# Kernel optimization log

Measured on AMD Instinct MI355X. Metric: run time of the kernel, lower is better.

## Reference

```python
import jax, jax.numpy as jnp
import numpy as np

B, T, D_IN, P, Q, D_OUT = 128, 1024, 64, 128, 2, 64


def _lstm_layer(x, w_ih, w_hh, b):
    """One LSTM layer, batch_first. x: [B,T,Din], w_ih: [4P,Din], w_hh: [4P,P], b: [4P].
    PyTorch gate order: i, f, g, o."""
    # Precompute input contribution for all timesteps (the big, parallel GEMM).
    gx = jnp.einsum('btd,gd->btg', x, w_ih) + b          # [B,T,4P]
    gx_t = jnp.swapaxes(gx, 0, 1)                        # [T,B,4P] for scan
    p = w_hh.shape[1]
    h0 = jnp.zeros((x.shape[0], p), dtype=x.dtype)
    c0 = jnp.zeros((x.shape[0], p), dtype=x.dtype)

    def step(carry, g_in):
        h, c = carry
        g = g_in + h @ w_hh.T                            # [B,4P]
        i, f, gg, o = jnp.split(g, 4, axis=-1)
        i = jax.nn.sigmoid(i)
        f = jax.nn.sigmoid(f)
        gg = jnp.tanh(gg)
        o = jax.nn.sigmoid(o)
        c = f * c + i * gg
        h = o * jnp.tanh(c)
        return (h, c), h

    _, hs = jax.lax.scan(step, (h0, c0), gx_t)           # hs: [T,B,P]
    return jnp.swapaxes(hs, 0, 1)                        # [B,T,P]


def setup_inputs() -> dict:
    key = jax.random.key(0)
    ks = jax.random.split(key, 8)
    x = jax.random.normal(ks[0], (B, T, D_IN), dtype=jnp.float32)
    # weight_ih: kaiming-normal-ish; weight_hh: orthogonal-ish (random normal is a fine stand-in
    # numerically; init distribution doesn't change the math being tested).
    w_ih0 = jax.random.normal(ks[1], (4 * P, D_IN), dtype=jnp.float32) * (1.0 / np.sqrt(D_IN))
    w_hh0 = jax.random.normal(ks[2], (4 * P, P), dtype=jnp.float32) * (1.0 / np.sqrt(P))
    w_ih1 = jax.random.normal(ks[3], (4 * P, P), dtype=jnp.float32) * (1.0 / np.sqrt(P))
    w_hh1 = jax.random.normal(ks[4], (4 * P, P), dtype=jnp.float32) * (1.0 / np.sqrt(P))
    # biases initialized to zero in the original (bias_ih + bias_hh folded into one per layer
    # would be equivalent math; keep both for faithfulness)
    b_ih = jnp.zeros((Q, 4 * P), dtype=jnp.float32)
    b_hh = jnp.zeros((Q, 4 * P), dtype=jnp.float32)
    fc_w = jax.random.normal(ks[5], (D_OUT, P), dtype=jnp.float32) * np.sqrt(2.0 / P)
    fc_b = jnp.zeros((D_OUT,), dtype=jnp.float32)
    return {"x": x, "w_ih0": w_ih0, "w_hh0": w_hh0, "w_ih1": w_ih1, "w_hh1": w_hh1,
            "b_ih": b_ih, "b_hh": b_hh, "fc_w": fc_w, "fc_b": fc_b}


def reference(x, w_ih0, w_hh0, w_ih1, w_hh1, b_ih, b_hh, fc_w, fc_b):
    h = _lstm_layer(x, w_ih0, w_hh0, b_ih[0] + b_hh[0])   # layer 0: [B,T,P]
    h = _lstm_layer(h, w_ih1, w_hh1, b_ih[1] + b_hh[1])   # layer 1: [B,T,P]
    return jnp.einsum('btp,op->bto', h, fc_w) + fc_b      # [B,T,D_OUT]
```

## Files before the change

kernel.cpp:

```cpp
#include <hip/hip_runtime.h>

#define NT 1024
#define RINGS 256

typedef _Float16 half8 __attribute__((ext_vector_type(8)));
typedef _Float16 half4 __attribute__((ext_vector_type(4)));
typedef float f32x4 __attribute__((ext_vector_type(4)));
typedef unsigned long long u64;
struct U2 { u64 a, b; };

#ifndef __has_builtin
#define __has_builtin(x) 0
#endif

__device__ __forceinline__ f32x4 MFMA(half8 a, half8 b, f32x4 c) {
  return __builtin_amdgcn_mfma_f32_16x16x32_f16(a, b, c, 0, 0, 0);
}
__device__ __forceinline__ float exp2h(float x) {
#if __has_builtin(__builtin_amdgcn_exp2f)
  return __builtin_amdgcn_exp2f(x);
#else
  return exp2f(x);
#endif
}
__device__ __forceinline__ float sigf(float x) {
  return __builtin_amdgcn_rcpf(1.0f + exp2h(x * -1.44269504f));
}
__device__ __forceinline__ float tanhf2(float x) {
  float t = __builtin_amdgcn_rcpf(1.0f + exp2h(x * 2.88539008f));
  return fmaf(-2.0f, t, 1.0f);
}
__device__ __forceinline__ half8 cvt8(float4 c0, float4 c1) {
  half8 hv;
  hv[0] = (_Float16)c0.x; hv[1] = (_Float16)c0.y;
  hv[2] = (_Float16)c0.z; hv[3] = (_Float16)c0.w;
  hv[4] = (_Float16)c1.x; hv[5] = (_Float16)c1.y;
  hv[6] = (_Float16)c1.z; hv[7] = (_Float16)c1.w;
  return hv;
}
__device__ __forceinline__ half8 ldring(const _Float16* p) {
  const u64* q = (const u64*)p;
  U2 uu;
  uu.a = __hip_atomic_load(q, __ATOMIC_RELAXED, __HIP_MEMORY_SCOPE_AGENT);
  uu.b = __hip_atomic_load(q + 1, __ATOMIC_RELAXED, __HIP_MEMORY_SCOPE_AGENT);
  return __builtin_bit_cast(half8, uu);
}
__device__ __forceinline__ unsigned wpoll(unsigned* p, unsigned tgt,
                                          unsigned cached, int l) {
  unsigned c = cached;
  while (c < tgt) {
    unsigned pv = 0;
    if (l == 0)
      pv = __hip_atomic_load(p, __ATOMIC_ACQUIRE, __HIP_MEMORY_SCOPE_AGENT);
    c = (unsigned)__builtin_amdgcn_readfirstlane((int)pv);
    if (c < tgt) __builtin_amdgcn_s_sleep(2);
  }
  return c;
}

__global__ __launch_bounds__(256) void prep_x(const float* __restrict__ x,
                                              _Float16* __restrict__ Xf) {
  int t0 = blockIdx.x * 256 + threadIdx.x;
  int l = t0 & 63;
  int fid = t0 >> 6;
  int kt = fid & 1;
  int t = (fid >> 1) & (NT - 1);
  int g = fid >> 11;
  int bt = g * 16 + (l & 15);
  int kb = kt * 32 + (l >> 4) * 4;
  const float* src = x + ((size_t)bt * NT + (size_t)t) * 64 + kb;
  float4 v0 = *(const float4*)src;
  float4 v1 = *(const float4*)(src + 16);
  *(half8*)(Xf + (size_t)fid * 512 + l * 8) = cvt8(v0, v1);
}

__global__ __launch_bounds__(512, 1) void lstm_main(
    const float* __restrict__ wih0, const float* __restrict__ whh0,
    const float* __restrict__ wih1, const float* __restrict__ whh1,
    const float* __restrict__ bih, const float* __restrict__ bhh,
    const float* __restrict__ fcw, const float* __restrict__ fcb,
    const _Float16* __restrict__ Xf, _Float16* __restrict__ ringH0,
    unsigned* __restrict__ flags, float* __restrict__ out) {
  const int tid = threadIdx.x;
  const int w = tid >> 6, l = tid & 63;
  const int n = l & 15, lg = l >> 4;
  const bool producer = blockIdx.x < 8;
  const int g = blockIdx.x & 7;

  __shared__ _Float16 hfr[2][4][64][8];
  __shared__ _Float16 fcl[4][4][64][8];

  _Float16* ringG = ringH0 + (size_t)g * RINGS * 2048;
  unsigned* prog = flags + g * 16;
  unsigned* cons = flags + (8 + g) * 16;
  const half8 hz = {0, 0, 0, 0, 0, 0, 0, 0};

  if (producer) {
    half8 A[4][6];
    f32x4 bias[4];
#pragma unroll
    for (int q = 0; q < 4; ++q) {
      int row = (w + 8 * q) * 16 + n;
#pragma unroll
      for (int kt = 0; kt < 2; ++kt) {
        const float* wp = wih0 + (size_t)row * 64 + kt * 32 + lg * 4;
        A[q][kt] = cvt8(*(const float4*)wp, *(const float4*)(wp + 16));
      }
#pragma unroll
      for (int kt = 0; kt < 4; ++kt) {
        const float* wp = whh0 + (size_t)row * 128 + kt * 32 + lg * 4;
        A[q][2 + kt] = cvt8(*(const float4*)wp, *(const float4*)(wp + 16));
      }
      int rb = (w + 8 * q) * 16 + lg * 4;
      f32x4 bv;
#pragma unroll
      for (int r = 0; r < 4; ++r) bv[r] = bih[rb + r] + bhh[rb + r];
      bias[q] = bv;
    }
    if (tid < 256) ((half8*)&hfr[1][0][0][0])[tid] = hz;
    const _Float16* XfG = Xf + (size_t)g * NT * 1024;
    half8 x0 = *(const half8*)(XfG + l * 8);
    half8 x1 = *(const half8*)(XfG + 512 + l * 8);
    f32x4 cst = {0.f, 0.f, 0.f, 0.f};
    unsigned Cc = 0;
    __syncthreads();
    for (int s = 0; s < NT; ++s) {
      half8 xn0, xn1;
      if (s + 1 < NT) {
        const _Float16* p = XfG + (size_t)(s + 1) * 1024 + l * 8;
        xn0 = *(const half8*)p;
        xn1 = *(const half8*)(p + 512);
      }
      if (s >= 224 && (s & 31) == 0)
        Cc = wpoll(cons, (unsigned)(s - 192), Cc, l);
      const int rdk = (s + 1) & 1;
      half8 b2 = *(const half8*)&hfr[rdk][0][l][0];
      half8 b3 = *(const half8*)&hfr[rdk][1][l][0];
      half8 b4 = *(const half8*)&hfr[rdk][2][l][0];
      half8 b5 = *(const half8*)&hfr[rdk][3][l][0];
      f32x4 xc0 = {0.f, 0.f, 0.f, 0.f}, xc1 = xc0, xc2 = xc0, xc3 = xc0;
      xc0 = MFMA(A[0][0], x0, xc0); xc1 = MFMA(A[1][0], x0, xc1);
      xc2 = MFMA(A[2][0], x0, xc2); xc3 = MFMA(A[3][0], x0, xc3);
      xc0 = MFMA(A[0][1], x1, xc0); xc1 = MFMA(A[1][1], x1, xc1);
      xc2 = MFMA(A[2][1], x1, xc2); xc3 = MFMA(A[3][1], x1, xc3);
      f32x4 hc0 = bias[0], hc1 = bias[1], hc2 = bias[2], hc3 = bias[3];
      hc0 = MFMA(A[0][2], b2, hc0); hc1 = MFMA(A[1][2], b2, hc1);
      hc2 = MFMA(A[2][2], b2, hc2); hc3 = MFMA(A[3][2], b2, hc3);
      hc0 = MFMA(A[0][3], b3, hc0); hc1 = MFMA(A[1][3], b3, hc1);
      hc2 = MFMA(A[2][3], b3, hc2); hc3 = MFMA(A[3][3], b3, hc3);
      hc0 = MFMA(A[0][4], b4, hc0); hc1 = MFMA(A[1][4], b4, hc1);
      hc2 = MFMA(A[2][4], b4, hc2); hc3 = MFMA(A[3][4], b4, hc3);
      hc0 = MFMA(A[0][5], b5, hc0); hc1 = MFMA(A[1][5], b5, hc1);
      hc2 = MFMA(A[2][5], b5, hc2); hc3 = MFMA(A[3][5], b5, hc3);
      f32x4 acc0 = hc0 + xc0, acc1 = hc1 + xc1;
      f32x4 acc2 = hc2 + xc2, acc3 = hc3 + xc3;
      half4 hh;
#pragma unroll
      for (int r = 0; r < 4; ++r) {
        float iv = sigf(acc0[r]), fv = sigf(acc1[r]);
        float gv = tanhf2(acc2[r]), ov = sigf(acc3[r]);
        cst[r] = fv * cst[r] + iv * gv;
        hh[r] = (_Float16)(ov * tanhf2(cst[r]));
      }
      *(half4*)&hfr[s & 1][w >> 1][l][(w & 1) << 2] = hh;
      {
        u64 uh = __builtin_bit_cast(u64, hh);
        __hip_atomic_store(
            (u64*)(ringG + (size_t)(s & (RINGS - 1)) * 2048 +
                   (w >> 1) * 512 + l * 8 + (w & 1) * 4),
            uh, __ATOMIC_RELAXED, __HIP_MEMORY_SCOPE_AGENT);
      }
      asm volatile("s_waitcnt lgkmcnt(0)" ::: "memory");
      __builtin_amdgcn_sched_barrier(0);
      __builtin_amdgcn_s_barrier();
      __builtin_amdgcn_sched_barrier(0);
      if ((s & 31) == 31) {
        asm volatile("s_waitcnt vmcnt(0)" ::: "memory");
        __builtin_amdgcn_sched_barrier(0);
        __builtin_amdgcn_s_barrier();
        __builtin_amdgcn_sched_barrier(0);
        if (tid == 0)
          __hip_atomic_store(prog, (unsigned)(s + 1), __ATOMIC_RELEASE,
                             __HIP_MEMORY_SCOPE_AGENT);
      }
      x0 = xn0;
      x1 = xn1;
    }
  } else {
    half8 A[4][8];
    f32x4 bias[4], fcbv = {0.f, 0.f, 0.f, 0.f};
#pragma unroll
    for (int q = 0; q < 4; ++q) {
      int row = (w + 8 * q) * 16 + n;
#pragma unroll
      for (int kt = 0; kt < 4; ++kt) {
        const float* wp = wih1 + (size_t)row * 128 + kt * 32 + lg * 4;
        A[q][kt] = cvt8(*(const float4*)wp, *(const float4*)(wp + 16));
      }
#pragma unroll
      for (int kt = 0; kt < 4; ++kt) {
        const float* wp = whh1 + (size_t)row * 128 + kt * 32 + lg * 4;
        A[q][4 + kt] = cvt8(*(const float4*)wp, *(const float4*)(wp + 16));
      }
      int rb = (w + 8 * q) * 16 + lg * 4;
      f32x4 bv;
#pragma unroll
      for (int r = 0; r < 4; ++r)
        bv[r] = bih[512 + rb + r] + bhh[512 + rb + r];
      bias[q] = bv;
    }
    if (w < 4) {
      int frow = (w << 4) + n;
#pragma unroll
      for (int kt = 0; kt < 4; ++kt) {
        const float* wp = fcw + (size_t)frow * 128 + kt * 32 + lg * 4;
        *(half8*)&fcl[w][kt][l][0] =
            cvt8(*(const float4*)wp, *(const float4*)(wp + 16));
      }
      fcbv = *(const f32x4*)(fcb + (w << 4) + lg * 4);
    }
    if (tid < 256) ((half8*)&hfr[1][0][0][0])[tid] = hz;
    float* outG = out + (size_t)((g << 4) + n) * NT * 64 + (w << 4) + lg * 4;
    f32x4 cst = {0.f, 0.f, 0.f, 0.f};
    __syncthreads();
    unsigned Pc = wpoll(prog, 2u, 0u, l);
    half8 hA0 = ldring(ringG + l * 8);
    half8 hA1 = ldring(ringG + 512 + l * 8);
    half8 hA2 = ldring(ringG + 1024 + l * 8);
    half8 hA3 = ldring(ringG + 1536 + l * 8);
    const _Float16* rb1 = ringG + 2048 + l * 8;
    half8 hB0 = ldring(rb1);
    half8 hB1 = ldring(rb1 + 512);
    half8 hB2 = ldring(rb1 + 1024);
    half8 hB3 = ldring(rb1 + 1536);

#define CSTEP(T, C0, C1, C2, C3)                                               \
  {                                                                            \
    const int rdk_ = ((T) + 1) & 1;                                            \
    half8 b4 = *(const half8*)&hfr[rdk_][0][l][0];                             \
    half8 b5 = *(const half8*)&hfr[rdk_][1][l][0];                             \
    half8 b6 = *(const half8*)&hfr[rdk_][2][l][0];                             \
    half8 b7 = *(const half8*)&hfr[rdk_][3][l][0];                             \
                      \
    f32x4 ic0 = {0.f, 0.f, 0.f, 0.f}, ic1 = ic0, ic2 = ic0, ic3 = ic0;         \
    ic0 = MFMA(A[0][0], C0, ic0); ic1 = MFMA(A[1][0], C0, ic1);                \
    ic2 = MFMA(A[2][0], C0, ic2); ic3 = MFMA(A[3][0], C0, ic3);                \
    ic0 = MFMA(A[0][1], C1, ic0); ic1 = MFMA(A[1][1], C1, ic1);                \
    ic2 = MFMA(A[2][1], C1, ic2); ic3 = MFMA(A[3][1], C1, ic3);                \
    ic0 = MFMA(A[0][2], C2, ic0); ic1 = MFMA(A[1][2], C2, ic1);                \
    ic2 = MFMA(A[2][2], C2, ic2); ic3 = MFMA(A[3][2], C2, ic3);                \
    ic0 = MFMA(A[0][3], C3, ic0); ic1 = MFMA(A[1][3], C3, ic1);                \
    ic2 = MFMA(A[2][3], C3, ic2); ic3 = MFMA(A[3][3], C3, ic3);                \
    if ((T) + 2 < NT) {    \
      Pc = wpoll(prog, (unsigned)((T) + 3), Pc, l);                            \
      const _Float16* rb_ =                                                    \
          ringG + (size_t)(((T) + 2) & (RINGS - 1)) * 2048 + l * 8;            \
      C0 = ldring(rb_);        C1 = ldring(rb_ + 512);                         \
      C2 = ldring(rb_ + 1024); C3 = ldring(rb_ + 1536);                        \
    }                                                                          \
                                                   \
    f32x4 hc0 = bias[0], hc1 = bias[1], hc2 = bias[2], hc3 = bias[3];          \
    hc0 = MFMA(A[0][4], b4, hc0); hc1 = MFMA(A[1][4], b4, hc1);                \
    hc2 = MFMA(A[2][4], b4, hc2); hc3 = MFMA(A[3][4], b4, hc3);                \
    hc0 = MFMA(A[0][5], b5, hc0); hc1 = MFMA(A[1][5], b5, hc1);                \
    hc2 = MFMA(A[2][5], b5, hc2); hc3 = MFMA(A[3][5], b5, hc3);                \
    hc0 = MFMA(A[0][6], b6, hc0); hc1 = MFMA(A[1][6], b6, hc1);                \
    hc2 = MFMA(A[2][6], b6, hc2); hc3 = MFMA(A[3][6], b6, hc3);                \
    hc0 = MFMA(A[0][7], b7, hc0); hc1 = MFMA(A[1][7], b7, hc1);                \
    hc2 = MFMA(A[2][7], b7, hc2); hc3 = MFMA(A[3][7], b7, hc3);                \
    if (w < 4) {                           \
      half8 f0 = *(const half8*)&fcl[w][0][l][0];                              \
      half8 f1 = *(const half8*)&fcl[w][1][l][0];                              \
      half8 f2 = *(const half8*)&fcl[w][2][l][0];                              \
      half8 f3 = *(const half8*)&fcl[w][3][l][0];                              \
      f32x4 afc = fcbv;                                                        \
      afc = MFMA(f0, b4, afc); afc = MFMA(f1, b5, afc);                        \
      afc = MFMA(f2, b6, afc); afc = MFMA(f3, b7, afc);                        \
      if ((T) >= 1) *(f32x4*)(outG + (size_t)((T) - 1) * 64) = afc;            \
    }                                                                          \
    f32x4 acc0 = hc0 + ic0, acc1 = hc1 + ic1;                                  \
    f32x4 acc2 = hc2 + ic2, acc3 = hc3 + ic3;                                  \
    half4 hh;                                                                  \
    _Pragma("unroll")                                                          \
    for (int r = 0; r < 4; ++r) {                                              \
      float iv = sigf(acc0[r]), fv = sigf(acc1[r]);                            \
      float gv = tanhf2(acc2[r]), ov = sigf(acc3[r]);                          \
      cst[r] = fv * cst[r] + iv * gv;                                          \
      hh[r] = (_Float16)(ov * tanhf2(cst[r]));                                 \
    }                                                                          \
    *(half4*)&hfr[(T) & 1][w >> 1][l][(w & 1) << 2] = hh;                      \
    if (tid == 0 && ((T) & 31) == 0)                                           \
      __hip_atomic_store(cons, (unsigned)(T), __ATOMIC_RELAXED,                \
                         __HIP_MEMORY_SCOPE_AGENT);                            \
    asm volatile("s_waitcnt lgkmcnt(0)" ::: "memory");                         \
    __builtin_amdgcn_sched_barrier(0);                                         \
    __builtin_amdgcn_s_barrier();             \
    __builtin_amdgcn_sched_barrier(0);                                         \
  }

    for (int t = 0; t < NT; t += 2) {
      CSTEP(t, hA0, hA1, hA2, hA3);
      CSTEP(t + 1, hB0, hB1, hB2, hB3);
    }
#undef CSTEP
    {
      half8 b4 = *(const half8*)&hfr[(NT + 1) & 1][0][l][0];
      half8 b5 = *(const half8*)&hfr[(NT + 1) & 1][1][l][0];
      half8 b6 = *(const half8*)&hfr[(NT + 1) & 1][2][l][0];
      half8 b7 = *(const half8*)&hfr[(NT + 1) & 1][3][l][0];
      if (w < 4) {
        half8 f0 = *(const half8*)&fcl[w][0][l][0];
        half8 f1 = *(const half8*)&fcl[w][1][l][0];
        half8 f2 = *(const half8*)&fcl[w][2][l][0];
        half8 f3 = *(const half8*)&fcl[w][3][l][0];
        f32x4 afc = fcbv;
        afc = MFMA(f0, b4, afc); afc = MFMA(f1, b5, afc);
        afc = MFMA(f2, b6, afc); afc = MFMA(f3, b7, afc);
        *(f32x4*)(outG + (size_t)(NT - 1) * 64) = afc;
      }
    }
  }
}

extern "C" void kernel_launch(void* const* d_in, const int* in_sizes, int n_in,
                              void* d_out, int out_size, void* d_ws, size_t ws_size,
                              hipStream_t stream) {
  const float* x     = (const float*)d_in[0];
  const float* w_ih0 = (const float*)d_in[1];
  const float* w_hh0 = (const float*)d_in[2];
  const float* w_ih1 = (const float*)d_in[3];
  const float* w_hh1 = (const float*)d_in[4];
  const float* b_ih  = (const float*)d_in[5];
  const float* b_hh  = (const float*)d_in[6];
  const float* fc_w  = (const float*)d_in[7];
  const float* fc_b  = (const float*)d_in[8];

  _Float16* Xf   = (_Float16*)d_ws;
  _Float16* ring = (_Float16*)((char*)d_ws + (16u << 20));
  unsigned* flags = (unsigned*)((char*)d_ws + (24u << 20));

  hipMemsetAsync(flags, 0, 4096, stream);
  prep_x<<<4096, 256, 0, stream>>>(x, Xf);
  lstm_main<<<16, 512, 0, stream>>>(w_ih0, w_hh0, w_ih1, w_hh1, b_ih, b_hh,
                                    fc_w, fc_b, Xf, ring, flags,
                                    (float*)d_out);
}
```

Baseline: 1.337 ms.

## Split layer-1 input projection into separate workgroups pipelined via global ring

Adds a third role of 8 workgroups that computes layer-1's input projection (W_ih1·h0 + bias) from the layer-0 ring and writes fp32 gate pre-activations to a new global ring. The layer-1 recurrent workgroups then only do the W_hh1 MFMAs plus FC on the serial critical path. Progress flags are published every 16 steps instead of 32, and ring loads switch from relaxed atomics to plain loads. This shortens the per-step dependency chain of layer 1 at the cost of an extra global round-trip, more flag polling and 8 more workgroups.

```diff
diff --git a/kernel.cpp b/kernel.cpp
--- a/kernel.cpp
+++ b/kernel.cpp
@@ -1,13 +1,13 @@
 #include <hip/hip_runtime.h>
 
 #define NT 1024
-#define RINGS 256
+#define H0S 256
+#define GS 64
 
 typedef _Float16 half8 __attribute__((ext_vector_type(8)));
 typedef _Float16 half4 __attribute__((ext_vector_type(4)));
 typedef float f32x4 __attribute__((ext_vector_type(4)));
 typedef unsigned long long u64;
-struct U2 { u64 a, b; };
 
 #ifndef __has_builtin
 #define __has_builtin(x) 0
@@ -37,13 +37,6 @@
   hv[4] = (_Float16)c1.x; hv[5] = (_Float16)c1.y;
   hv[6] = (_Float16)c1.z; hv[7] = (_Float16)c1.w;
   return hv;
-}
-__device__ __forceinline__ half8 ldring(const _Float16* p) {
-  const u64* q = (const u64*)p;
-  U2 uu;
-  uu.a = __hip_atomic_load(q, __ATOMIC_RELAXED, __HIP_MEMORY_SCOPE_AGENT);
-  uu.b = __hip_atomic_load(q + 1, __ATOMIC_RELAXED, __HIP_MEMORY_SCOPE_AGENT);
-  return __builtin_bit_cast(half8, uu);
 }
 __device__ __forceinline__ unsigned wpoll(unsigned* p, unsigned tgt,
                                           unsigned cached, int l) {
@@ -57,6 +50,18 @@
   }
   return c;
 }
+
+#define DRAIN_BARRIER()                              \
+  asm volatile("s_waitcnt vmcnt(0)" ::: "memory");   \
+  __builtin_amdgcn_sched_barrier(0);                 \
+  __builtin_amdgcn_s_barrier();                      \
+  __builtin_amdgcn_sched_barrier(0)
+
+#define LGKM_BARRIER()                               \
+  asm volatile("s_waitcnt lgkmcnt(0)" ::: "memory"); \
+  __builtin_amdgcn_sched_barrier(0);                 \
+  __builtin_amdgcn_s_barrier();                      \
+  __builtin_amdgcn_sched_barrier(0)
 
 __global__ __launch_bounds__(256) void prep_x(const float* __restrict__ x,
                                               _Float16* __restrict__ Xf) {
@@ -79,23 +84,26 @@
     const float* __restrict__ wih1, const float* __restrict__ whh1,
     const float* __restrict__ bih, const float* __restrict__ bhh,
     const float* __restrict__ fcw, const float* __restrict__ fcb,
-    const _Float16* __restrict__ Xf, _Float16* __restrict__ ringH0,
-    unsigned* __restrict__ flags, float* __restrict__ out) {
+    const _Float16* __restrict__ Xf, _Float16* __restrict__ h0R,
+    float* __restrict__ gyR, unsigned* __restrict__ flags,
+    float* __restrict__ out) {
   const int tid = threadIdx.x;
   const int w = tid >> 6, l = tid & 63;
   const int n = l & 15, lg = l >> 4;
-  const bool producer = blockIdx.x < 8;
+  const int role = blockIdx.x >> 3;
   const int g = blockIdx.x & 7;
 
   __shared__ _Float16 hfr[2][4][64][8];
   __shared__ _Float16 fcl[4][4][64][8];
 
-  _Float16* ringG = ringH0 + (size_t)g * RINGS * 2048;
-  unsigned* prog = flags + g * 16;
-  unsigned* cons = flags + (8 + g) * 16;
+  _Float16* h0G = h0R + (size_t)g * H0S * 2048;
+  float* gyG = gyR + (size_t)g * GS * 8192;
+  unsigned* pP  = flags + (0 * 8 + g) * 16;
+  unsigned* pXY = flags + (1 * 8 + g) * 16;
+  unsigned* pY  = flags + (2 * 8 + g) * 16;
   const half8 hz = {0, 0, 0, 0, 0, 0, 0, 0};
 
-  if (producer) {
+  if (role == 0) {
     half8 A[4][6];
     f32x4 bias[4];
 #pragma unroll
@@ -122,7 +130,7 @@
     half8 x0 = *(const half8*)(XfG + l * 8);
     half8 x1 = *(const half8*)(XfG + 512 + l * 8);
     f32x4 cst = {0.f, 0.f, 0.f, 0.f};
-    unsigned Cc = 0;
+    unsigned XYp = 0;
     __syncthreads();
     for (int s = 0; s < NT; ++s) {
       half8 xn0, xn1;
@@ -132,82 +140,127 @@
         xn1 = *(const half8*)(p + 512);
       }
       if (s >= 224 && (s & 31) == 0)
-        Cc = wpoll(cons, (unsigned)(s - 192), Cc, l);
+        XYp = wpoll(pXY, (unsigned)(s - 192), XYp, l);
       const int rdk = (s + 1) & 1;
       half8 b2 = *(const half8*)&hfr[rdk][0][l][0];
       half8 b3 = *(const half8*)&hfr[rdk][1][l][0];
       half8 b4 = *(const half8*)&hfr[rdk][2][l][0];
       half8 b5 = *(const half8*)&hfr[rdk][3][l][0];
-      f32x4 xc0 = {0.f, 0.f, 0.f, 0.f}, xc1 = xc0, xc2 = xc0, xc3 = xc0;
-      xc0 = MFMA(A[0][0], x0, xc0); xc1 = MFMA(A[1][0], x0, xc1);
-      xc2 = MFMA(A[2][0], x0, xc2); xc3 = MFMA(A[3][0], x0, xc3);
-      xc0 = MFMA(A[0][1], x1, xc0); xc1 = MFMA(A[1][1], x1, xc1);
-      xc2 = MFMA(A[2][1], x1, xc2); xc3 = MFMA(A[3][1], x1, xc3);
-      f32x4 hc0 = bias[0], hc1 = bias[1], hc2 = bias[2], hc3 = bias[3];
-      hc0 = MFMA(A[0][2], b2, hc0); hc1 = MFMA(A[1][2], b2, hc1);
-      hc2 = MFMA(A[2][2], b2, hc2); hc3 = MFMA(A[3][2], b2, hc3);
-      hc0 = MFMA(A[0][3], b3, hc0); hc1 = MFMA(A[1][3], b3, hc1);
-      hc2 = MFMA(A[2][3], b3, hc2); hc3 = MFMA(A[3][3], b3, hc3);
-      hc0 = MFMA(A[0][4], b4, hc0); hc1 = MFMA(A[1][4], b4, hc1);
-      hc2 = MFMA(A[2][4], b4, hc2); hc3 = MFMA(A[3][4], b4, hc3);
-      hc0 = MFMA(A[0][5], b5, hc0); hc1 = MFMA(A[1][5], b5, hc1);
-      hc2 = MFMA(A[2][5], b5, hc2); hc3 = MFMA(A[3][5], b5, hc3);
-      f32x4 acc0 = hc0 + xc0, acc1 = hc1 + xc1;
-      f32x4 acc2 = hc2 + xc2, acc3 = hc3 + xc3;
+      f32x4 a0 = bias[0], a1 = bias[1], a2 = bias[2], a3 = bias[3];
+      a0 = MFMA(A[0][0], x0, a0); a1 = MFMA(A[1][0], x0, a1);
+      a2 = MFMA(A[2][0], x0, a2); a3 = MFMA(A[3][0], x0, a3);
+      a0 = MFMA(A[0][1], x1, a0); a1 = MFMA(A[1][1], x1, a1);
+      a2 = MFMA(A[2][1], x1, a2); a3 = MFMA(A[3][1], x1, a3);
+      a0 = MFMA(A[0][2], b2, a0); a1 = MFMA(A[1][2], b2, a1);
+      a2 = MFMA(A[2][2], b2, a2); a3 = MFMA(A[3][2], b2, a3);
+      a0 = MFMA(A[0][3], b3, a0); a1 = MFMA(A[1][3], b3, a1);
+      a2 = MFMA(A[2][3], b3, a2); a3 = MFMA(A[3][3], b3, a3);
+      a0 = MFMA(A[0][4], b4, a0); a1 = MFMA(A[1][4], b4, a1);
+      a2 = MFMA(A[2][4], b4, a2); a3 = MFMA(A[3][4], b4, a3);
+      a0 = MFMA(A[0][5], b5, a0); a1 = MFMA(A[1][5], b5, a1);
+      a2 = MFMA(A[2][5], b5, a2); a3 = MFMA(A[3][5], b5, a3);
       half4 hh;
 #pragma unroll
       for (int r = 0; r < 4; ++r) {
-        float iv = sigf(acc0[r]), fv = sigf(acc1[r]);
-        float gv = tanhf2(acc2[r]), ov = sigf(acc3[r]);
+        float iv = sigf(a0[r]), fv = sigf(a1[r]);
+        float gv = tanhf2(a2[r]), ov = sigf(a3[r]);
         cst[r] = fv * cst[r] + iv * gv;
         hh[r] = (_Float16)(ov * tanhf2(cst[r]));
       }
       *(half4*)&hfr[s & 1][w >> 1][l][(w & 1) << 2] = hh;
-      {
-        u64 uh = __builtin_bit_cast(u64, hh);
-        __hip_atomic_store(
-            (u64*)(ringG + (size_t)(s & (RINGS - 1)) * 2048 +
-                   (w >> 1) * 512 + l * 8 + (w & 1) * 4),
-            uh, __ATOMIC_RELAXED, __HIP_MEMORY_SCOPE_AGENT);
-      }
-      asm volatile("s_waitcnt lgkmcnt(0)" ::: "memory");
-      __builtin_amdgcn_sched_barrier(0);
-      __builtin_amdgcn_s_barrier();
-      __builtin_amdgcn_sched_barrier(0);
-      if ((s & 31) == 31) {
-        asm volatile("s_waitcnt vmcnt(0)" ::: "memory");
-        __builtin_amdgcn_sched_barrier(0);
-        __builtin_amdgcn_s_barrier();
-        __builtin_amdgcn_sched_barrier(0);
+      *(u64*)(h0G + (size_t)(s & (H0S - 1)) * 2048 + (w >> 1) * 512 + l * 8 +
+              (w & 1) * 4) = __builtin_bit_cast(u64, hh);
+      LGKM_BARRIER();
+      if ((s & 15) == 15) {
+        DRAIN_BARRIER();
         if (tid == 0)
-          __hip_atomic_store(prog, (unsigned)(s + 1), __ATOMIC_RELEASE,
+          __hip_atomic_store(pP, (unsigned)(s + 1), __ATOMIC_RELEASE,
                              __HIP_MEMORY_SCOPE_AGENT);
       }
       x0 = xn0;
       x1 = xn1;
     }
-  } else {
-    half8 A[4][8];
-    f32x4 bias[4], fcbv = {0.f, 0.f, 0.f, 0.f};
+  } else if (role == 1) {
+    half8 Ai[4][4];
+    f32x4 b1v[4];
 #pragma unroll
     for (int q = 0; q < 4; ++q) {
       int row = (w + 8 * q) * 16 + n;
 #pragma unroll
       for (int kt = 0; kt < 4; ++kt) {
         const float* wp = wih1 + (size_t)row * 128 + kt * 32 + lg * 4;
-        A[q][kt] = cvt8(*(const float4*)wp, *(const float4*)(wp + 16));
-      }
+        Ai[q][kt] = cvt8(*(const float4*)wp, *(const float4*)(wp + 16));
+      }
+      int rb = (w + 8 * q) * 16 + lg * 4;
+      f32x4 bv;
+#pragma unroll
+      for (int r = 0; r < 4; ++r)
+        bv[r] = bih[512 + rb + r] + bhh[512 + rb + r];
+      b1v[q] = bv;
+    }
+    unsigned Pp = wpoll(pP, 2u, 0u, l), Yp = 0;
+    const _Float16* hp0 = h0G + l * 8;
+    half8 hA0 = *(const half8*)hp0;
+    half8 hA1 = *(const half8*)(hp0 + 512);
+    half8 hA2 = *(const half8*)(hp0 + 1024);
+    half8 hA3 = *(const half8*)(hp0 + 1536);
+    const _Float16* hp1 = h0G + 2048 + l * 8;
+    half8 hB0 = *(const half8*)hp1;
+    half8 hB1 = *(const half8*)(hp1 + 512);
+    half8 hB2 = *(const half8*)(hp1 + 1024);
+    half8 hB3 = *(const half8*)(hp1 + 1536);
+
+#define XSTEP(U, H0_, H1_, H2_, H3_)                                           \
+  {                                                                            \
+    f32x4 c0 = b1v[0], c1 = b1v[1], c2 = b1v[2], c3 = b1v[3];                  \
+    c0 = MFMA(Ai[0][0], H0_, c0); c1 = MFMA(Ai[1][0], H0_, c1);                \
+    c2 = MFMA(Ai[2][0], H0_, c2); c3 = MFMA(Ai[3][0], H0_, c3);                \
+    c0 = MFMA(Ai[0][1], H1_, c0); c1 = MFMA(Ai[1][1], H1_, c1);                \
+    c2 = MFMA(Ai[2][1], H1_, c2); c3 = MFMA(Ai[3][1], H1_, c3);                \
+    c0 = MFMA(Ai[0][2], H2_, c0); c1 = MFMA(Ai[1][2], H2_, c1);                \
+    c2 = MFMA(Ai[2][2], H2_, c2); c3 = MFMA(Ai[3][2], H2_, c3);                \
+    c0 = MFMA(Ai[0][3], H3_, c0); c1 = MFMA(Ai[1][3], H3_, c1);                \
+    c2 = MFMA(Ai[2][3], H3_, c2); c3 = MFMA(Ai[3][3], H3_, c3);                \
+    float* gp = gyG + (size_t)((U) & (GS - 1)) * 8192;                         \
+    *(f32x4*)(gp + ((0 + w) * 64 + l) * 4) = c0;                               \
+    *(f32x4*)(gp + ((8 + w) * 64 + l) * 4) = c1;                               \
+    *(f32x4*)(gp + ((16 + w) * 64 + l) * 4) = c2;                              \
+    *(f32x4*)(gp + ((24 + w) * 64 + l) * 4) = c3;                              \
+    if ((U) + 2 < NT) {                \
+      Pp = wpoll(pP, (unsigned)((U) + 3), Pp, l);                              \
+      const _Float16* hp_ =                                                    \
+          h0G + (size_t)(((U) + 2) & (H0S - 1)) * 2048 + l * 8;                \
+      H0_ = *(const half8*)hp_;                                                \
+      H1_ = *(const half8*)(hp_ + 512);                                        \
+      H2_ = *(const half8*)(hp_ + 1024);                                       \
+      H3_ = *(const half8*)(hp_ + 1536);                                       \
+    }                                                                          \
+    if (((U) & 15) == 0 && (U) >= 48)       \
+      Yp = wpoll(pY, (unsigned)((U) - 40), Yp, l);                             \
+    if (((U) & 15) == 15) {                                                    \
+      DRAIN_BARRIER();                                                         \
+      if (tid == 0)                                                            \
+        __hip_atomic_store(pXY, (unsigned)((U) + 1), __ATOMIC_RELEASE,         \
+                           __HIP_MEMORY_SCOPE_AGENT);                          \
+    }                                                                          \
+  }
+
+    for (int u = 0; u < NT; u += 2) {
+      XSTEP(u, hA0, hA1, hA2, hA3);
+      XSTEP(u + 1, hB0, hB1, hB2, hB3);
+    }
+#undef XSTEP
+  } else {
+    half8 Ah[4][4];
+    f32x4 fcbv = {0.f, 0.f, 0.f, 0.f};
+#pragma unroll
+    for (int q = 0; q < 4; ++q) {
+      int row = (w + 8 * q) * 16 + n;
 #pragma unroll
       for (int kt = 0; kt < 4; ++kt) {
         const float* wp = whh1 + (size_t)row * 128 + kt * 32 + lg * 4;
-        A[q][4 + kt] = cvt8(*(const float4*)wp, *(const float4*)(wp + 16));
-      }
-      int rb = (w + 8 * q) * 16 + lg * 4;
-      f32x4 bv;
-#pragma unroll
-      for (int r = 0; r < 4; ++r)
-        bv[r] = bih[512 + rb + r] + bhh[512 + rb + r];
-      bias[q] = bv;
+        Ah[q][kt] = cvt8(*(const float4*)wp, *(const float4*)(wp + 16));
+      }
     }
     if (w < 4) {
       int frow = (w << 4) + n;
@@ -223,99 +276,85 @@
     float* outG = out + (size_t)((g << 4) + n) * NT * 64 + (w << 4) + lg * 4;
     f32x4 cst = {0.f, 0.f, 0.f, 0.f};
     __syncthreads();
-    unsigned Pc = wpoll(prog, 2u, 0u, l);
-    half8 hA0 = ldring(ringG + l * 8);
-    half8 hA1 = ldring(ringG + 512 + l * 8);
-    half8 hA2 = ldring(ringG + 1024 + l * 8);
-    half8 hA3 = ldring(ringG + 1536 + l * 8);
-    const _Float16* rb1 = ringG + 2048 + l * 8;
-    half8 hB0 = ldring(rb1);
-    half8 hB1 = ldring(rb1 + 512);
-    half8 hB2 = ldring(rb1 + 1024);
-    half8 hB3 = ldring(rb1 + 1536);
-
-#define CSTEP(T, C0, C1, C2, C3)                                               \
+    unsigned XYp = wpoll(pXY, 2u, 0u, l);
+    f32x4 gA0 = *(const f32x4*)(gyG + ((0 + w) * 64 + l) * 4);
+    f32x4 gA1 = *(const f32x4*)(gyG + ((8 + w) * 64 + l) * 4);
+    f32x4 gA2 = *(const f32x4*)(gyG + ((16 + w) * 64 + l) * 4);
+    f32x4 gA3 = *(const f32x4*)(gyG + ((24 + w) * 64 + l) * 4);
+    const float* g1p = gyG + 8192;
+    f32x4 gB0 = *(const f32x4*)(g1p + ((0 + w) * 64 + l) * 4);
+    f32x4 gB1 = *(const f32x4*)(g1p + ((8 + w) * 64 + l) * 4);
+    f32x4 gB2 = *(const f32x4*)(g1p + ((16 + w) * 64 + l) * 4);
+    f32x4 gB3 = *(const f32x4*)(g1p + ((24 + w) * 64 + l) * 4);
+
+#define YSTEP(T, G0, G1, G2, G3)                                               \
   {                                                                            \
     const int rdk_ = ((T) + 1) & 1;                                            \
-    half8 b4 = *(const half8*)&hfr[rdk_][0][l][0];                             \
-    half8 b5 = *(const half8*)&hfr[rdk_][1][l][0];                             \
-    half8 b6 = *(const half8*)&hfr[rdk_][2][l][0];                             \
-    half8 b7 = *(const half8*)&hfr[rdk_][3][l][0];                             \
-                      \
-    f32x4 ic0 = {0.f, 0.f, 0.f, 0.f}, ic1 = ic0, ic2 = ic0, ic3 = ic0;         \
-    ic0 = MFMA(A[0][0], C0, ic0); ic1 = MFMA(A[1][0], C0, ic1);                \
-    ic2 = MFMA(A[2][0], C0, ic2); ic3 = MFMA(A[3][0], C0, ic3);                \
-    ic0 = MFMA(A[0][1], C1, ic0); ic1 = MFMA(A[1][1], C1, ic1);                \
-    ic2 = MFMA(A[2][1], C1, ic2); ic3 = MFMA(A[3][1], C1, ic3);                \
-    ic0 = MFMA(A[0][2], C2, ic0); ic1 = MFMA(A[1][2], C2, ic1);                \
-    ic2 = MFMA(A[2][2], C2, ic2); ic3 = MFMA(A[3][2], C2, ic3);                \
-    ic0 = MFMA(A[0][3], C3, ic0); ic1 = MFMA(A[1][3], C3, ic1);                \
-    ic2 = MFMA(A[2][3], C3, ic2); ic3 = MFMA(A[3][3], C3, ic3);                \
-    if ((T) + 2 < NT) {    \
-      Pc = wpoll(prog, (unsigned)((T) + 3), Pc, l);                            \
-      const _Float16* rb_ =                                                    \
-          ringG + (size_t)(((T) + 2) & (RINGS - 1)) * 2048 + l * 8;            \
-      C0 = ldring(rb_);        C1 = ldring(rb_ + 512);                         \
-      C2 = ldring(rb_ + 1024); C3 = ldring(rb_ + 1536);                        \
-    }                                                                          \
-                                                   \
-    f32x4 hc0 = bias[0], hc1 = bias[1], hc2 = bias[2], hc3 = bias[3];          \
-    hc0 = MFMA(A[0][4], b4, hc0); hc1 = MFMA(A[1][4], b4, hc1);                \
-    hc2 = MFMA(A[2][4], b4, hc2); hc3 = MFMA(A[3][4], b4, hc3);                \
-    hc0 = MFMA(A[0][5], b5, hc0); hc1 = MFMA(A[1][5], b5, hc1);                \
-    hc2 = MFMA(A[2][5], b5, hc2); hc3 = MFMA(A[3][5], b5, hc3);                \
-    hc0 = MFMA(A[0][6], b6, hc0); hc1 = MFMA(A[1][6], b6, hc1);                \
-    hc2 = MFMA(A[2][6], b6, hc2); hc3 = MFMA(A[3][6], b6, hc3);                \
-    hc0 = MFMA(A[0][7], b7, hc0); hc1 = MFMA(A[1][7], b7, hc1);                \
-    hc2 = MFMA(A[2][7], b7, hc2); hc3 = MFMA(A[3][7], b7, hc3);                \
-    if (w < 4) {                           \
+    half8 b0 = *(const half8*)&hfr[rdk_][0][l][0];                             \
+    half8 b1 = *(const half8*)&hfr[rdk_][1][l][0];                             \
+    half8 b2 = *(const half8*)&hfr[rdk_][2][l][0];                             \
+    half8 b3 = *(const half8*)&hfr[rdk_][3][l][0];                             \
+    f32x4 c0 = G0, c1 = G1, c2 = G2, c3 = G3;                                  \
+    c0 = MFMA(Ah[0][0], b0, c0); c1 = MFMA(Ah[1][0], b0, c1);                  \
+    c2 = MFMA(Ah[2][0], b0, c2); c3 = MFMA(Ah[3][0], b0, c3);                  \
+    c0 = MFMA(Ah[0][1], b1, c0); c1 = MFMA(Ah[1][1], b1, c1);                  \
+    c2 = MFMA(Ah[2][1], b1, c2); c3 = MFMA(Ah[3][1], b1, c3);                  \
+    c0 = MFMA(Ah[0][2], b2, c0); c1 = MFMA(Ah[1][2], b2, c1);                  \
+    c2 = MFMA(Ah[2][2], b2, c2); c3 = MFMA(Ah[3][2], b2, c3);                  \
+    c0 = MFMA(Ah[0][3], b3, c0); c1 = MFMA(Ah[1][3], b3, c1);                  \
+    c2 = MFMA(Ah[2][3], b3, c2); c3 = MFMA(Ah[3][3], b3, c3);                  \
+    if (w < 4) {                                            \
       half8 f0 = *(const half8*)&fcl[w][0][l][0];                              \
       half8 f1 = *(const half8*)&fcl[w][1][l][0];                              \
       half8 f2 = *(const half8*)&fcl[w][2][l][0];                              \
       half8 f3 = *(const half8*)&fcl[w][3][l][0];                              \
       f32x4 afc = fcbv;                                                        \
-      afc = MFMA(f0, b4, afc); afc = MFMA(f1, b5, afc);                        \
-      afc = MFMA(f2, b6, afc); afc = MFMA(f3, b7, afc);                        \
+      afc = MFMA(f0, b0, afc); afc = MFMA(f1, b1, afc);                        \
+      afc = MFMA(f2, b2, afc); afc = MFMA(f3, b3, afc);                        \
       if ((T) >= 1) *(f32x4*)(outG + (size_t)((T) - 1) * 64) = afc;            \
     }                                                                          \
-    f32x4 acc0 = hc0 + ic0, acc1 = hc1 + ic1;                                  \
-    f32x4 acc2 = hc2 + ic2, acc3 = hc3 + ic3;                                  \
+    if ((T) + 2 < NT) {                                  \
+      XYp = wpoll(pXY, (unsigned)((T) + 3), XYp, l);                           \
+      const float* gp_ = gyG + (size_t)(((T) + 2) & (GS - 1)) * 8192;          \
+      G0 = *(const f32x4*)(gp_ + ((0 + w) * 64 + l) * 4);                      \
+      G1 = *(const f32x4*)(gp_ + ((8 + w) * 64 + l) * 4);                      \
+      G2 = *(const f32x4*)(gp_ + ((16 + w) * 64 + l) * 4);                     \
+      G3 = *(const f32x4*)(gp_ + ((24 + w) * 64 + l) * 4);                     \
+    }                                                                          \
     half4 hh;                                                                  \
     _Pragma("unroll")                                                          \
     for (int r = 0; r < 4; ++r) {                                              \
-      float iv = sigf(acc0[r]), fv = sigf(acc1[r]);                            \
-      float gv = tanhf2(acc2[r]), ov = sigf(acc3[r]);                          \
+      float iv = sigf(c0[r]), fv = sigf(c1[r]);                                \
+      float gv = tanhf2(c2[r]), ov = sigf(c3[r]);                              \
       cst[r] = fv * cst[r] + iv * gv;                                          \
       hh[r] = (_Float16)(ov * tanhf2(cst[r]));                                 \
     }                                                                          \
     *(half4*)&hfr[(T) & 1][w >> 1][l][(w & 1) << 2] = hh;                      \
-    if (tid == 0 && ((T) & 31) == 0)                                           \
-      __hip_atomic_store(cons, (unsigned)(T), __ATOMIC_RELAXED,                \
+    LGKM_BARRIER();                                                            \
+    if (((T) & 15) == 15 && tid == 0)                                          \
+      __hip_atomic_store(pY, (unsigned)((T) + 1), __ATOMIC_RELAXED,            \
                          __HIP_MEMORY_SCOPE_AGENT);                            \
-    asm volatile("s_waitcnt lgkmcnt(0)" ::: "memory");                         \
-    __builtin_amdgcn_sched_barrier(0);                                         \
-    __builtin_amdgcn_s_barrier();             \
-    __builtin_amdgcn_sched_barrier(0);                                         \
   }
 
     for (int t = 0; t < NT; t += 2) {
-      CSTEP(t, hA0, hA1, hA2, hA3);
-      CSTEP(t + 1, hB0, hB1, hB2, hB3);
-    }
-#undef CSTEP
+      YSTEP(t, gA0, gA1, gA2, gA3);
+      YSTEP(t + 1, gB0, gB1, gB2, gB3);
+    }
+#undef YSTEP
     {
-      half8 b4 = *(const half8*)&hfr[(NT + 1) & 1][0][l][0];
-      half8 b5 = *(const half8*)&hfr[(NT + 1) & 1][1][l][0];
-      half8 b6 = *(const half8*)&hfr[(NT + 1) & 1][2][l][0];
-      half8 b7 = *(const half8*)&hfr[(NT + 1) & 1][3][l][0];
+      const int rdk = (NT + 1) & 1;
+      half8 b0 = *(const half8*)&hfr[rdk][0][l][0];
+      half8 b1 = *(const half8*)&hfr[rdk][1][l][0];
+      half8 b2 = *(const half8*)&hfr[rdk][2][l][0];
+      half8 b3 = *(const half8*)&hfr[rdk][3][l][0];
       if (w < 4) {
         half8 f0 = *(const half8*)&fcl[w][0][l][0];
         half8 f1 = *(const half8*)&fcl[w][1][l][0];
         half8 f2 = *(const half8*)&fcl[w][2][l][0];
         half8 f3 = *(const half8*)&fcl[w][3][l][0];
         f32x4 afc = fcbv;
-        afc = MFMA(f0, b4, afc); afc = MFMA(f1, b5, afc);
-        afc = MFMA(f2, b6, afc); afc = MFMA(f3, b7, afc);
+        afc = MFMA(f0, b0, afc); afc = MFMA(f1, b1, afc);
+        afc = MFMA(f2, b2, afc); afc = MFMA(f3, b3, afc);
         *(f32x4*)(outG + (size_t)(NT - 1) * 64) = afc;
       }
     }
@@ -335,13 +374,14 @@
   const float* fc_w  = (const float*)d_in[7];
   const float* fc_b  = (const float*)d_in[8];
 
-  _Float16* Xf   = (_Float16*)d_ws;
-  _Float16* ring = (_Float16*)((char*)d_ws + (16u << 20));
-  unsigned* flags = (unsigned*)((char*)d_ws + (24u << 20));
-
-  hipMemsetAsync(flags, 0, 4096, stream);
+  _Float16* Xf  = (_Float16*)d_ws;
+  _Float16* h0R = (_Float16*)((char*)d_ws + (16u << 20));
+  float* gyR    = (float*)((char*)d_ws + (24u << 20));
+  unsigned* flags = (unsigned*)((char*)d_ws + (40u << 20));
+
+  (void)hipMemsetAsync(flags, 0, 4096, stream);
   prep_x<<<4096, 256, 0, stream>>>(x, Xf);
-  lstm_main<<<16, 512, 0, stream>>>(w_ih0, w_hh0, w_ih1, w_hh1, b_ih, b_hh,
-                                    fc_w, fc_b, Xf, ring, flags,
+  lstm_main<<<24, 512, 0, stream>>>(w_ih0, w_hh0, w_ih1, w_hh1, b_ih, b_hh,
+                                    fc_w, fc_b, Xf, h0R, gyR, flags,
                                     (float*)d_out);
 }
```

Result: faster. 1.256 ms (-6.1%).
